# Kernel optimization log

Measured on AMD Instinct MI355X. Metric: run time of the kernel, lower is better.

Reference implementation:

```python
import jax, jax.numpy as jnp
import numpy as np

HEADS = 8
HEAD_DIM = 32
PRE_H = 32
PRE_W = 32
SCALE = HEAD_DIM ** (-0.5)


def _relative_indices(H, W):
    # Faithful to torch loop: out[p, q] = (gy[q]-y_p+H)*W + (gx[q]-x_p+W)
    gy, gx = np.meshgrid(np.arange(H), np.arange(W), indexing='ij')
    gy = gy.reshape(-1)
    gx = gx.reshape(-1)
    idx = (gy[None, :] - gy[:, None] + H) * W + (gx[None, :] - gx[:, None] + W)
    return idx.astype(np.int32)  # [HW, HW]


def setup_inputs() -> dict:
    key = jax.random.key(0)
    ks = jax.random.split(key, 7)
    b, c, H, W = 16, 256, PRE_H, PRE_W
    dim = HEADS * HEAD_DIM  # 256
    x = jax.random.normal(ks[0], (b, c, H, W), dtype=jnp.float32)
    # nn.Linear weights: [out_features, in_features]
    Wq = jax.random.normal(ks[1], (dim, c), dtype=jnp.float32) * 0.02
    Wk = jax.random.normal(ks[2], (dim, c), dtype=jnp.float32) * 0.02
    Wv = jax.random.normal(ks[3], (dim, c), dtype=jnp.float32) * 0.02
    Wo = jax.random.normal(ks[4], (c, dim), dtype=jnp.float32) * 0.02
    bo = jax.random.normal(ks[5], (c,), dtype=jnp.float32) * 0.02
    rel_bias = jax.random.normal(ks[6], (HEADS, (2 * PRE_H - 1) * (2 * PRE_W - 1)), dtype=jnp.float32)
    rel_idx = jnp.asarray(_relative_indices(PRE_H, PRE_W))
    return {"x": x, "Wq": Wq, "Wk": Wk, "Wv": Wv, "Wo": Wo, "bo": bo,
            "rel_bias": rel_bias, "rel_idx": rel_idx}


def reference(x, Wq, Wk, Wv, Wo, bo, rel_bias, rel_idx):
    b, c, H, W = x.shape
    n = H * W
    h, d = HEADS, HEAD_DIM
    # b c h w -> b (h w) c
    xt = x.reshape(b, c, n).transpose(0, 2, 1)
    q = (xt @ Wq.T).reshape(b, n, h, d).transpose(0, 2, 1, 3)  # b h n d
    k = (xt @ Wk.T).reshape(b, n, h, d).transpose(0, 2, 1, 3)
    v = (xt @ Wv.T).reshape(b, n, h, d).transpose(0, 2, 1, 3)
    k = k * SCALE
    # gathered relative bias: [h, n, n]
    bias = rel_bias[:, rel_idx]
    attn = jnp.einsum('bhnd,bhmd->bhnm', q, k) + bias[None]
    attn = jax.nn.softmax(attn, axis=-1)
    out = jnp.einsum('bhnm,bhmd->bhnd', attn, v)
    out = out.transpose(0, 2, 1, 3).reshape(b, n, h * d)  # b n (h d)
    out = out @ Wo.T + bo
    # b (h w) c -> b c h w
    return out.transpose(0, 2, 1).reshape(b, c, H, W)
```

## Files before the change

### kernel.cpp

```cpp
#include <hip/hip_runtime.h>

#define HEADS 8
#define HDIM 32
#define NTOK 1024
#define CDIM 256
#define BATCH 16
#define ATT_SCALE 0.17677669529663687f
#define L2E 1.4426950408889634f
#define BSTR 1544
#define XROW 66

typedef __attribute__((ext_vector_type(8))) short bf16x8;
typedef __attribute__((ext_vector_type(4))) float f32x4;

__device__ __forceinline__ unsigned short f2bf(float f) {
    unsigned int u = __float_as_uint(f);
    return (unsigned short)((u + 0x7fffu + ((u >> 16) & 1u)) >> 16);
}

__device__ __forceinline__ unsigned cvt_pk_bf16(float lo, float hi) {
    unsigned r;
    asm("v_cvt_pk_bf16_f32 %0, %1, %2" : "=v"(r) : "v"(lo), "v"(hi));
    return r;
}

__global__ __launch_bounds__(256) void prepw_kernel(
    const float* __restrict__ Wq, const float* __restrict__ Wk,
    const float* __restrict__ Wv, const float* __restrict__ Wo,
    unsigned short* __restrict__ w16)
{
    const int t = threadIdx.x;
    const int which = blockIdx.y;
    const float* src = (which == 0) ? Wq : ((which == 1) ? Wk : ((which == 2) ? Wv : Wo));
    const float scale = (which == 1) ? (ATT_SCALE * L2E) : 1.0f;
    const int base = (blockIdx.x * 256 + t) * 16;
    #pragma unroll
    for (int i = 0; i < 4; ++i) {
        const int idx = base + i * 4;
        float4 v = *(const float4*)&src[idx];
        union { unsigned short h[4]; uint2 u; } pk;
        pk.h[0] = f2bf(v.x * scale); pk.h[1] = f2bf(v.y * scale);
        pk.h[2] = f2bf(v.z * scale); pk.h[3] = f2bf(v.w * scale);
        *(uint2*)&w16[(size_t)which * 65536 + idx] = pk.u;
    }
}

__global__ __launch_bounds__(1024, 4) void qkv_kernel(
    const float* __restrict__ x,
    const unsigned short* __restrict__ w16,
    unsigned short* __restrict__ q16,
    unsigned short* __restrict__ k16,
    unsigned short* __restrict__ v16)
{
    __shared__ __align__(16) unsigned char smem[65536];
    float (*lx)[32 * XROW] = (float(*)[32 * XROW])smem;
    unsigned short* bufA = (unsigned short*)smem;
    unsigned short* bufB = (unsigned short*)(smem + 32768);

    const int id  = blockIdx.x;
    const int b   = (id & 7) * 2 + (id >> 7);
    const int t16 = (id >> 3) & 15;

    const int t = threadIdx.x, wid = t >> 6, lane = t & 63;
    const int g = lane >> 4, ln = lane & 15;
    const int h = wid & 7, tgrp = wid >> 3;
    const int tok0 = t16 * 64;
    const int trl  = tgrp * 32;
    const int tr   = tok0 + trl;

    const float* xb = x + (size_t)b * CDIM * NTOK;
    const unsigned short* wqh = w16 + (size_t)(h * 32) * CDIM;
    const unsigned short* wkh = w16 + 65536 + (size_t)(h * 32) * CDIM;
    const unsigned short* wvh = w16 + 2 * 65536 + (size_t)(h * 32) * CDIM;

    const int scc = t >> 5, sl2 = (t & 31) * 2;

    f32x4 aq[2][2], ak[2][2], av[2][2];
    #pragma unroll
    for (int m = 0; m < 2; ++m)
        #pragma unroll
        for (int n = 0; n < 2; ++n) {
            aq[m][n] = (f32x4){0.f, 0.f, 0.f, 0.f};
            ak[m][n] = (f32x4){0.f, 0.f, 0.f, 0.f};
            av[n][m] = (f32x4){0.f, 0.f, 0.f, 0.f};
        }

    {
        const float2 v = *(const float2*)&xb[(size_t)scc * NTOK + tok0 + sl2];
        *(float2*)&lx[0][scc * XROW + sl2] = v;
    }
    __syncthreads();

    #pragma unroll
    for (int ci = 0; ci < 8; ++ci) {
        const int cur = ci & 1;
        const int kt = ci * 32;
        if (ci < 7) {
            const float2 v = *(const float2*)&xb[(size_t)(kt + 32 + scc) * NTOK + tok0 + sl2];
            *(float2*)&lx[cur ^ 1][scc * XROW + sl2] = v;
        }
        bf16x8 xf[2];
        #pragma unroll
        for (int m = 0; m < 2; ++m) {
            const float* col = &lx[cur][(size_t)(g * 8) * XROW + trl + m * 16 + ln];
            union { unsigned u4[4]; bf16x8 v; } pk;
            #pragma unroll
            for (int p = 0; p < 4; ++p)
                pk.u4[p] = cvt_pk_bf16(col[(2 * p) * XROW], col[(2 * p + 1) * XROW]);
            xf[m] = pk.v;
        }
        bf16x8 wqf[2], wkf[2], wvf[2];
        #pragma unroll
        for (int n = 0; n < 2; ++n) {
            wqf[n] = *(const bf16x8*)&wqh[(size_t)(n * 16 + ln) * CDIM + kt + g * 8];
            wkf[n] = *(const bf16x8*)&wkh[(size_t)(n * 16 + ln) * CDIM + kt + g * 8];
            wvf[n] = *(const bf16x8*)&wvh[(size_t)(n * 16 + ln) * CDIM + kt + g * 8];
        }
        #pragma unroll
        for (int m = 0; m < 2; ++m)
            #pragma unroll
            for (int n = 0; n < 2; ++n) {
                aq[m][n] = __builtin_amdgcn_mfma_f32_16x16x32_bf16(xf[m], wqf[n], aq[m][n], 0, 0, 0);
                ak[m][n] = __builtin_amdgcn_mfma_f32_16x16x32_bf16(xf[m], wkf[n], ak[m][n], 0, 0, 0);
                av[n][m] = __builtin_amdgcn_mfma_f32_16x16x32_bf16(wvf[n], xf[m], av[n][m], 0, 0, 0);
            }
        __syncthreads();
    }

    #pragma unroll
    for (int m = 0; m < 2; ++m)
        #pragma unroll
        for (int n = 0; n < 2; ++n) {
            const int lhi = (2 * n + (ln >> 3)) * 16 + (m * 2 + (g >> 1)) * 4;
            unsigned short* dst = &bufA[(h * 4 + tgrp * 2 + (g & 1)) * 512 + (ln & 7)];
            #pragma unroll
            for (int r = 0; r < 4; ++r)
                dst[(lhi + r) * 8] = f2bf(ak[m][n][r]);
        }
    __syncthreads();

    #pragma unroll
    for (int uu = 0; uu < 2; ++uu) {
        const int u = t + uu * 1024;
        const int hu = u >> 8, off = u & 255;
        uint4 vv = *(const uint4*)&bufA[hu * 2048 + off * 8];
        *(uint4*)&k16[(size_t)(b * 8 + hu) * 32768 + t16 * 2048 + off * 8] = vv;
    }
    #pragma unroll
    for (int n = 0; n < 2; ++n) {
        const int fl = tgrp * 2 + n;
        #pragma unroll
        for (int m = 0; m < 2; ++m) {
            const int lnb = (m * 2 + (ln >> 3)) * 16 + g * 4;
            unsigned short* dst = &bufB[(h * 4 + fl) * 512 + (ln & 7)];
            #pragma unroll
            for (int r = 0; r < 4; ++r)
                dst[(lnb + r) * 8] = f2bf(av[n][m][r]);
        }
    }
    __syncthreads();

    #pragma unroll
    for (int uu = 0; uu < 2; ++uu) {
        const int u = t + uu * 1024;
        const int hu = u >> 8, off = u & 255;
        uint4 vv = *(const uint4*)&bufB[hu * 2048 + off * 8];
        *(uint4*)&v16[(size_t)(b * 8 + hu) * 32768 + t16 * 2048 + off * 8] = vv;
    }
    #pragma unroll
    for (int m = 0; m < 2; ++m)
        #pragma unroll
        for (int n = 0; n < 2; ++n)
            #pragma unroll
            for (int r = 0; r < 4; ++r)
                bufA[(trl + m * 16 + g * 4 + r) * 256 + h * 32 + n * 16 + ln] = f2bf(aq[m][n][r]);
    __syncthreads();

    #pragma unroll
    for (int uu = 0; uu < 2; ++uu) {
        const int u = t + uu * 1024;
        *(uint4*)&q16[((size_t)(b * NTOK + tok0)) * 256 + u * 8] = *(const uint4*)&bufA[u * 8];
    }
}

__global__ __launch_bounds__(1024, 4) void attn_kernel(
    const unsigned short* __restrict__ q16,
    const unsigned short* __restrict__ k16,
    const unsigned short* __restrict__ v16,
    const float* __restrict__ rel_bias,
    unsigned short* __restrict__ ao16)
{
    __shared__ __align__(16) unsigned char smem[65536 + 65536 + BSTR * 4 * 4];
    unsigned short* k_s   = (unsigned short*)smem;
    unsigned short* v_s   = (unsigned short*)(smem + 65536);
    float*          bias4 = (float*)(smem + 131072);

    const int id   = blockIdx.x;
    const int bh_i = (id & 7) * 16 + (id >> 4);
    const int half = (id >> 3) & 1;
    const int b = bh_i >> 3, h = bh_i & 7;

    const int t = threadIdx.x, wid = t >> 6, lane = t & 63;
    const int g = lane >> 4, ln = lane & 15;
    const int qb = half * 512 + wid * 32;

    const unsigned short* kbh = k16 + (size_t)(b * 8 + h) * 32768;
    const unsigned short* vbh = v16 + (size_t)(b * 8 + h) * 32768;

    bf16x8 sk[4], sv[4];
    #pragma unroll
    for (int j = 0; j < 4; ++j) {
        const int f = wid * 4 + j;
        sk[j] = *(const bf16x8*)&kbh[(size_t)f * 512 + lane * 8];
        sv[j] = *(const bf16x8*)&vbh[(size_t)f * 512 + lane * 8];
    }
    const bf16x8 aq0 = *(const bf16x8*)&q16[((size_t)(b * NTOK + qb + ln) * 8 + h) * 32 + g * 8];
    const bf16x8 aq1 = *(const bf16x8*)&q16[((size_t)(b * NTOK + qb + 16 + ln) * 8 + h) * 32 + g * 8];

    {
        const int START = 544 - 512 * half;
        const float* brow = rel_bias + (size_t)h * 3969;
        for (int i = t; i < 1540; i += 1024) {
            #pragma unroll
            for (int a = 0; a < 4; ++a)
                bias4[a * BSTR + i] = brow[START + a + i] * L2E;
        }
    }

    #pragma unroll
    for (int j = 0; j < 4; ++j) {
        const int f = wid * 4 + j;
        *(bf16x8*)&k_s[(size_t)f * 512 + lane * 8] = sk[j];
        *(bf16x8*)&v_s[(size_t)f * 512 + lane * 8] = sv[j];
    }

    __syncthreads();

    const int boffL = 512 + 8 * g - wid * 32 - ln;
    const int ba = boffL & 3;
    const float* bb = &bias4[ba * BSTR + (boffL - ba)];
    const unsigned short* kfp = k_s + lane * 8;
    const unsigned short* vfp = v_s + lane * 8;

    f32x4 o00 = {0.f,0.f,0.f,0.f}, o01 = {0.f,0.f,0.f,0.f};
    f32x4 o10 = {0.f,0.f,0.f,0.f}, o11 = {0.f,0.f,0.f,0.f};
    f32x4 ls0 = {0.f,0.f,0.f,0.f}, ls1 = {0.f,0.f,0.f,0.f};
    const short one_bf = (short)0x3F80;
    const bf16x8 ones = {one_bf,one_bf,one_bf,one_bf,one_bf,one_bf,one_bf,one_bf};

    bf16x8 kf0 = *(const bf16x8*)&kfp[0];
    bf16x8 kf1 = *(const bf16x8*)&kfp[512];
    f32x4  cA0 = *(const f32x4*)&bb[0];
    f32x4  cA1 = *(const f32x4*)&bb[4];
    f32x4  cB0 = *(const f32x4*)&bb[-16];
    f32x4  cB1 = *(const f32x4*)&bb[-12];

    for (int kb = 0; kb < NTOK; kb += 32) {
        const int fi = (kb >> 5) * 2;
        const bf16x8 vA0 = *(const bf16x8*)&vfp[fi * 512];
        const bf16x8 vA1 = *(const bf16x8*)&vfp[(fi + 1) * 512];
        const int kn = (kb + 32) & (NTOK - 1);
        const int fn = (kn >> 5) * 2;
        const bf16x8 nk0 = *(const bf16x8*)&kfp[fn * 512];
        const bf16x8 nk1 = *(const bf16x8*)&kfp[(fn + 1) * 512];
        const f32x4  nA0 = *(const f32x4*)&bb[kn];
        const f32x4  nA1 = *(const f32x4*)&bb[kn + 4];
        const f32x4  nB0 = *(const f32x4*)&bb[kn - 16];
        const f32x4  nB1 = *(const f32x4*)&bb[kn - 12];

        __builtin_amdgcn_s_setprio(1);
        f32x4 s00 = __builtin_amdgcn_mfma_f32_16x16x32_bf16(kf0, aq0, cA0, 0, 0, 0);
        f32x4 s01 = __builtin_amdgcn_mfma_f32_16x16x32_bf16(kf1, aq0, cA1, 0, 0, 0);
        f32x4 s10 = __builtin_amdgcn_mfma_f32_16x16x32_bf16(kf0, aq1, cB0, 0, 0, 0);
        f32x4 s11 = __builtin_amdgcn_mfma_f32_16x16x32_bf16(kf1, aq1, cB1, 0, 0, 0);
        __builtin_amdgcn_s_setprio(0);

        union { unsigned u4[4]; bf16x8 v; } ap0, ap1;
        ap0.u4[0] = cvt_pk_bf16(__builtin_amdgcn_exp2f(s00[0]), __builtin_amdgcn_exp2f(s00[1]));
        ap0.u4[1] = cvt_pk_bf16(__builtin_amdgcn_exp2f(s00[2]), __builtin_amdgcn_exp2f(s00[3]));
        ap0.u4[2] = cvt_pk_bf16(__builtin_amdgcn_exp2f(s01[0]), __builtin_amdgcn_exp2f(s01[1]));
        ap0.u4[3] = cvt_pk_bf16(__builtin_amdgcn_exp2f(s01[2]), __builtin_amdgcn_exp2f(s01[3]));
        ap1.u4[0] = cvt_pk_bf16(__builtin_amdgcn_exp2f(s10[0]), __builtin_amdgcn_exp2f(s10[1]));
        ap1.u4[1] = cvt_pk_bf16(__builtin_amdgcn_exp2f(s10[2]), __builtin_amdgcn_exp2f(s10[3]));
        ap1.u4[2] = cvt_pk_bf16(__builtin_amdgcn_exp2f(s11[0]), __builtin_amdgcn_exp2f(s11[1]));
        ap1.u4[3] = cvt_pk_bf16(__builtin_amdgcn_exp2f(s11[2]), __builtin_amdgcn_exp2f(s11[3]));

        __builtin_amdgcn_s_setprio(1);
        o00 = __builtin_amdgcn_mfma_f32_16x16x32_bf16(ap0.v, vA0, o00, 0, 0, 0);
        o01 = __builtin_amdgcn_mfma_f32_16x16x32_bf16(ap0.v, vA1, o01, 0, 0, 0);
        ls0 = __builtin_amdgcn_mfma_f32_16x16x32_bf16(ap0.v, ones, ls0, 0, 0, 0);
        o10 = __builtin_amdgcn_mfma_f32_16x16x32_bf16(ap1.v, vA0, o10, 0, 0, 0);
        o11 = __builtin_amdgcn_mfma_f32_16x16x32_bf16(ap1.v, vA1, o11, 0, 0, 0);
        ls1 = __builtin_amdgcn_mfma_f32_16x16x32_bf16(ap1.v, ones, ls1, 0, 0, 0);
        __builtin_amdgcn_s_setprio(0);

        kf0 = nk0; kf1 = nk1;
        cA0 = nA0; cA1 = nA1; cB0 = nB0; cB1 = nB1;
    }

    #pragma unroll
    for (int r = 0; r < 4; ++r) {
        float i0 = 1.f / ls0[r], i1 = 1.f / ls1[r];
        o00[r] *= i0; o01[r] *= i0;
        o10[r] *= i1; o11[r] *= i1;
    }

    __syncthreads();
    unsigned short (*otr)[32][40] = (unsigned short(*)[32][40])smem;
    #pragma unroll
    for (int r = 0; r < 4; ++r) {
        otr[wid][g * 4 + r][ln]           = f2bf(o00[r]);
        otr[wid][g * 4 + r][16 + ln]      = f2bf(o01[r]);
        otr[wid][16 + g * 4 + r][ln]      = f2bf(o10[r]);
        otr[wid][16 + g * 4 + r][16 + ln] = f2bf(o11[r]);
    }
    const int row = lane >> 1;
    const int ch  = (lane & 1) * 16;
    uint4 st0 = *(uint4*)&otr[wid][row][ch];
    uint4 st1 = *(uint4*)&otr[wid][row][ch + 8];
    unsigned short* dst = &ao16[((size_t)b * NTOK + qb + row) * CDIM + h * HDIM + ch];
    *(uint4*)dst     = st0;
    *(uint4*)&dst[8] = st1;
}

__global__ __launch_bounds__(256) void outproj_kernel(
    const unsigned short* __restrict__ ao16,
    const unsigned short* __restrict__ wo16,
    const float* __restrict__ bo,
    float* __restrict__ y)
{
    const int id   = blockIdx.x;
    const int b    = (id & 7) * 2 + ((id >> 3) & 1);
    const int rest = id >> 4;
    const int ct   = (rest & 3) * 64;
    const int pt   = (rest >> 2) * 128;
    const int t = threadIdx.x, wid = t >> 6, lane = t & 63;
    const int g = lane >> 4, ln = lane & 15;
    const int cb2 = ct + (wid & 1) * 32;
    const int pb  = pt + (wid >> 1) * 64;
    const unsigned short* ab = ao16 + (size_t)b * NTOK * CDIM;

    f32x4 acc[2][4];
    #pragma unroll
    for (int n = 0; n < 2; ++n)
        #pragma unroll
        for (int m = 0; m < 4; ++m) acc[n][m] = (f32x4){0.f, 0.f, 0.f, 0.f};

    #pragma unroll
    for (int kt = 0; kt < CDIM; kt += 32) {
        bf16x8 aw[2], bx[4];
        #pragma unroll
        for (int n = 0; n < 2; ++n)
            aw[n] = *(const bf16x8*)&wo16[(size_t)(cb2 + n * 16 + ln) * CDIM + kt + g * 8];
        #pragma unroll
        for (int m = 0; m < 4; ++m)
            bx[m] = *(const bf16x8*)&ab[(size_t)(pb + m * 16 + ln) * CDIM + kt + g * 8];
        #pragma unroll
        for (int n = 0; n < 2; ++n)
            #pragma unroll
            for (int m = 0; m < 4; ++m)
                acc[n][m] = __builtin_amdgcn_mfma_f32_16x16x32_bf16(aw[n], bx[m], acc[n][m], 0, 0, 0);
    }
    #pragma unroll
    for (int n = 0; n < 2; ++n)
        #pragma unroll
        for (int r = 0; r < 4; ++r) {
            const int c = cb2 + n * 16 + g * 4 + r;
            const float bias = bo[c];
            #pragma unroll
            for (int m = 0; m < 4; ++m)
                y[((size_t)b * CDIM + c) * NTOK + pb + m * 16 + ln] = acc[n][m][r] + bias;
        }
}

extern "C" void kernel_launch(void* const* d_in, const int* in_sizes, int n_in,
                              void* d_out, int out_size, void* d_ws, size_t ws_size,
                              hipStream_t stream) {
    const float* x        = (const float*)d_in[0];
    const float* Wq       = (const float*)d_in[1];
    const float* Wk       = (const float*)d_in[2];
    const float* Wv       = (const float*)d_in[3];
    const float* Wo       = (const float*)d_in[4];
    const float* bo       = (const float*)d_in[5];
    const float* rel_bias = (const float*)d_in[6];
    (void)in_sizes; (void)n_in; (void)ws_size; (void)out_size;

    unsigned short* ws16 = (unsigned short*)d_ws;
    unsigned short* w16  = ws16;
    unsigned short* q16  = ws16 + 4 * 65536;
    unsigned short* k16  = q16 + (size_t)4 * 1024 * 1024;
    unsigned short* v16  = k16 + (size_t)4 * 1024 * 1024;
    unsigned short* ao16 = v16 + (size_t)4 * 1024 * 1024;
    float* y = (float*)d_out;

    prepw_kernel<<<dim3(16, 4), 256, 0, stream>>>(Wq, Wk, Wv, Wo, w16);
    qkv_kernel<<<256, 1024, 0, stream>>>(x, w16, q16, k16, v16);
    attn_kernel<<<256, 1024, 0, stream>>>(q16, k16, v16, rel_bias, ao16);
    outproj_kernel<<<512, 256, 0, stream>>>(ao16, w16 + 3 * 65536, bo, y);
}
```

Before: 160.9 us.

## Split attention keys across two wave groups, read K/V from global, merge partials

The attention kernel now launches 512 blocks, each covering a quarter of the queries for one (batch, head). Within a block, the 16 waves are split into two halves, and each half processes half of the key range. K and V are no longer staged in LDS; they are read directly from global memory and rely on cache. The two halves' partial outputs and row sums are merged through shared memory, which shrinks LDS use and raises launch_bounds occupancy to 8. The trade-offs are more global/L2 traffic for K/V, an extra reduction with two barriers, and half the waves sitting idle during the epilogue.

```diff
diff --git a/kernel.cpp b/kernel.cpp
--- a/kernel.cpp
+++ b/kernel.cpp
@@ -7,8 +7,8 @@
 #define BATCH 16
 #define ATT_SCALE 0.17677669529663687f
 #define L2E 1.4426950408889634f
-#define BSTR 1544
 #define XROW 66
+#define BSTRQ 1288
 
 typedef __attribute__((ext_vector_type(8))) short bf16x8;
 typedef __attribute__((ext_vector_type(4))) float f32x4;
@@ -183,64 +183,48 @@
     }
 }
 
-__global__ __launch_bounds__(1024, 4) void attn_kernel(
+__global__ __launch_bounds__(1024, 8) void attn_kernel(
     const unsigned short* __restrict__ q16,
     const unsigned short* __restrict__ k16,
     const unsigned short* __restrict__ v16,
     const float* __restrict__ rel_bias,
     unsigned short* __restrict__ ao16)
 {
-    __shared__ __align__(16) unsigned char smem[65536 + 65536 + BSTR * 4 * 4];
-    unsigned short* k_s   = (unsigned short*)smem;
-    unsigned short* v_s   = (unsigned short*)(smem + 65536);
-    float*          bias4 = (float*)(smem + 131072);
-
-    const int id   = blockIdx.x;
-    const int bh_i = (id & 7) * 16 + (id >> 4);
-    const int half = (id >> 3) & 1;
-    const int b = bh_i >> 3, h = bh_i & 7;
+    __shared__ __align__(16) unsigned char smem[49152 + 20480];
+    float* bias4 = (float*)smem;
+    float* part  = (float*)smem;
+    unsigned short (*otr)[32][40] = (unsigned short(*)[32][40])(smem + 49152);
+
+    const int id = blockIdx.x;
+    const int b  = (id & 7) * 2 + ((id >> 3) & 1);
+    const int h  = (id >> 4) & 7;
+    const int quarter = id >> 7;
 
     const int t = threadIdx.x, wid = t >> 6, lane = t & 63;
     const int g = lane >> 4, ln = lane & 15;
-    const int qb = half * 512 + wid * 32;
+    const int qg = wid & 7, kh = wid >> 3;
+    const int q0 = quarter * 256 + qg * 32;
 
     const unsigned short* kbh = k16 + (size_t)(b * 8 + h) * 32768;
     const unsigned short* vbh = v16 + (size_t)(b * 8 + h) * 32768;
 
-    bf16x8 sk[4], sv[4];
-    #pragma unroll
-    for (int j = 0; j < 4; ++j) {
-        const int f = wid * 4 + j;
-        sk[j] = *(const bf16x8*)&kbh[(size_t)f * 512 + lane * 8];
-        sv[j] = *(const bf16x8*)&vbh[(size_t)f * 512 + lane * 8];
-    }
-    const bf16x8 aq0 = *(const bf16x8*)&q16[((size_t)(b * NTOK + qb + ln) * 8 + h) * 32 + g * 8];
-    const bf16x8 aq1 = *(const bf16x8*)&q16[((size_t)(b * NTOK + qb + 16 + ln) * 8 + h) * 32 + g * 8];
+    const bf16x8 aq0 = *(const bf16x8*)&q16[((size_t)(b * NTOK + q0 + ln) * 8 + h) * 32 + g * 8];
+    const bf16x8 aq1 = *(const bf16x8*)&q16[((size_t)(b * NTOK + q0 + 16 + ln) * 8 + h) * 32 + g * 8];
 
     {
-        const int START = 544 - 512 * half;
+        const int S0 = 801 - 256 * quarter;
         const float* brow = rel_bias + (size_t)h * 3969;
-        for (int i = t; i < 1540; i += 1024) {
+        for (int i = t; i < 1279; i += 1024) {
             #pragma unroll
             for (int a = 0; a < 4; ++a)
-                bias4[a * BSTR + i] = brow[START + a + i] * L2E;
-        }
-    }
-
-    #pragma unroll
-    for (int j = 0; j < 4; ++j) {
-        const int f = wid * 4 + j;
-        *(bf16x8*)&k_s[(size_t)f * 512 + lane * 8] = sk[j];
-        *(bf16x8*)&v_s[(size_t)f * 512 + lane * 8] = sv[j];
-    }
-
-    __syncthreads();
-
-    const int boffL = 512 + 8 * g - wid * 32 - ln;
-    const int ba = boffL & 3;
-    const float* bb = &bias4[ba * BSTR + (boffL - ba)];
-    const unsigned short* kfp = k_s + lane * 8;
-    const unsigned short* vfp = v_s + lane * 8;
+                bias4[a * BSTRQ + i] = brow[S0 + a + i] * L2E;
+        }
+    }
+    __syncthreads();
+
+    const int offL = 255 + 8 * g - qg * 32 - ln;
+    const int ba = offL & 3;
+    const float* bb = &bias4[ba * BSTRQ + (offL - ba)];
 
     f32x4 o00 = {0.f,0.f,0.f,0.f}, o01 = {0.f,0.f,0.f,0.f};
     f32x4 o10 = {0.f,0.f,0.f,0.f}, o11 = {0.f,0.f,0.f,0.f};
@@ -248,21 +232,25 @@
     const short one_bf = (short)0x3F80;
     const bf16x8 ones = {one_bf,one_bf,one_bf,one_bf,one_bf,one_bf,one_bf,one_bf};
 
-    bf16x8 kf0 = *(const bf16x8*)&kfp[0];
-    bf16x8 kf1 = *(const bf16x8*)&kfp[512];
-    f32x4  cA0 = *(const f32x4*)&bb[0];
-    f32x4  cA1 = *(const f32x4*)&bb[4];
-    f32x4  cB0 = *(const f32x4*)&bb[-16];
-    f32x4  cB1 = *(const f32x4*)&bb[-12];
-
-    for (int kb = 0; kb < NTOK; kb += 32) {
-        const int fi = (kb >> 5) * 2;
-        const bf16x8 vA0 = *(const bf16x8*)&vfp[fi * 512];
-        const bf16x8 vA1 = *(const bf16x8*)&vfp[(fi + 1) * 512];
-        const int kn = (kb + 32) & (NTOK - 1);
-        const int fn = (kn >> 5) * 2;
-        const bf16x8 nk0 = *(const bf16x8*)&kfp[fn * 512];
-        const bf16x8 nk1 = *(const bf16x8*)&kfp[(fn + 1) * 512];
+    const int kk0 = kh * 512;
+    const int fb  = kh * 32;
+
+    bf16x8 kf0 = *(const bf16x8*)&kbh[(size_t)fb * 512 + lane * 8];
+    bf16x8 kf1 = *(const bf16x8*)&kbh[(size_t)(fb + 1) * 512 + lane * 8];
+    f32x4  cA0 = *(const f32x4*)&bb[kk0];
+    f32x4  cA1 = *(const f32x4*)&bb[kk0 + 4];
+    f32x4  cB0 = *(const f32x4*)&bb[kk0 - 16];
+    f32x4  cB1 = *(const f32x4*)&bb[kk0 - 12];
+
+    for (int kbl = 0; kbl < 512; kbl += 32) {
+        const int fi = fb + (kbl >> 5) * 2;
+        const bf16x8 vA0 = *(const bf16x8*)&vbh[(size_t)fi * 512 + lane * 8];
+        const bf16x8 vA1 = *(const bf16x8*)&vbh[(size_t)(fi + 1) * 512 + lane * 8];
+        const int knl = (kbl + 32) & 511;
+        const int kn  = kk0 + knl;
+        const int fn  = fb + (knl >> 5) * 2;
+        const bf16x8 nk0 = *(const bf16x8*)&kbh[(size_t)fn * 512 + lane * 8];
+        const bf16x8 nk1 = *(const bf16x8*)&kbh[(size_t)(fn + 1) * 512 + lane * 8];
         const f32x4  nA0 = *(const f32x4*)&bb[kn];
         const f32x4  nA1 = *(const f32x4*)&bb[kn + 4];
         const f32x4  nB0 = *(const f32x4*)&bb[kn - 16];
@@ -298,29 +286,45 @@
         cA0 = nA0; cA1 = nA1; cB0 = nB0; cB1 = nB1;
     }
 
-    #pragma unroll
-    for (int r = 0; r < 4; ++r) {
-        float i0 = 1.f / ls0[r], i1 = 1.f / ls1[r];
-        o00[r] *= i0; o01[r] *= i0;
-        o10[r] *= i1; o11[r] *= i1;
-    }
-
-    __syncthreads();
-    unsigned short (*otr)[32][40] = (unsigned short(*)[32][40])smem;
-    #pragma unroll
-    for (int r = 0; r < 4; ++r) {
-        otr[wid][g * 4 + r][ln]           = f2bf(o00[r]);
-        otr[wid][g * 4 + r][16 + ln]      = f2bf(o01[r]);
-        otr[wid][16 + g * 4 + r][ln]      = f2bf(o10[r]);
-        otr[wid][16 + g * 4 + r][16 + ln] = f2bf(o11[r]);
-    }
-    const int row = lane >> 1;
-    const int ch  = (lane & 1) * 16;
-    uint4 st0 = *(uint4*)&otr[wid][row][ch];
-    uint4 st1 = *(uint4*)&otr[wid][row][ch + 8];
-    unsigned short* dst = &ao16[((size_t)b * NTOK + qb + row) * CDIM + h * HDIM + ch];
-    *(uint4*)dst     = st0;
-    *(uint4*)&dst[8] = st1;
+    __syncthreads();
+
+    if (kh == 1) {
+        float* p = &part[((size_t)qg * 64 + lane) * 24];
+        *(f32x4*)&p[0]  = o00;  *(f32x4*)&p[4]  = o01;
+        *(f32x4*)&p[8]  = o10;  *(f32x4*)&p[12] = o11;
+        *(f32x4*)&p[16] = ls0;  *(f32x4*)&p[20] = ls1;
+    }
+    __syncthreads();
+
+    if (kh == 0) {
+        const float* p = &part[((size_t)qg * 64 + lane) * 24];
+        const f32x4 p00 = *(const f32x4*)&p[0],  p01 = *(const f32x4*)&p[4];
+        const f32x4 p10 = *(const f32x4*)&p[8],  p11 = *(const f32x4*)&p[12];
+        const f32x4 pl0 = *(const f32x4*)&p[16], pl1 = *(const f32x4*)&p[20];
+        #pragma unroll
+        for (int r = 0; r < 4; ++r) {
+            const float l0 = ls0[r] + pl0[r], l1 = ls1[r] + pl1[r];
+            const float i0 = 1.f / l0, i1 = 1.f / l1;
+            o00[r] = (o00[r] + p00[r]) * i0;
+            o01[r] = (o01[r] + p01[r]) * i0;
+            o10[r] = (o10[r] + p10[r]) * i1;
+            o11[r] = (o11[r] + p11[r]) * i1;
+        }
+        #pragma unroll
+        for (int r = 0; r < 4; ++r) {
+            otr[qg][g * 4 + r][ln]           = f2bf(o00[r]);
+            otr[qg][g * 4 + r][16 + ln]      = f2bf(o01[r]);
+            otr[qg][16 + g * 4 + r][ln]      = f2bf(o10[r]);
+            otr[qg][16 + g * 4 + r][16 + ln] = f2bf(o11[r]);
+        }
+        const int row = lane >> 1;
+        const int ch  = (lane & 1) * 16;
+        uint4 st0 = *(uint4*)&otr[qg][row][ch];
+        uint4 st1 = *(uint4*)&otr[qg][row][ch + 8];
+        unsigned short* dst = &ao16[((size_t)b * NTOK + q0 + row) * CDIM + h * HDIM + ch];
+        *(uint4*)dst     = st0;
+        *(uint4*)&dst[8] = st1;
+    }
 }
 
 __global__ __launch_bounds__(256) void outproj_kernel(
@@ -395,6 +399,6 @@
 
     prepw_kernel<<<dim3(16, 4), 256, 0, stream>>>(Wq, Wk, Wv, Wo, w16);
     qkv_kernel<<<256, 1024, 0, stream>>>(x, w16, q16, k16, v16);
-    attn_kernel<<<256, 1024, 0, stream>>>(q16, k16, v16, rel_bias, ao16);
+    attn_kernel<<<512, 1024, 0, stream>>>(q16, k16, v16, rel_bias, ao16);
     outproj_kernel<<<512, 256, 0, stream>>>(ao16, w16 + 3 * 65536, bo, y);
 }
```

New measurement: 385.7 us. +139.7%, slower.
